# Performance work log

Hardware: AMD Instinct MI355X
Metric: run time of the kernel (lower is better)

## Reference

```python
import jax, jax.numpy as jnp
import numpy as np

D = 128  # chunk_embSize

def _mlp_one_layer(x, W, b):
    # MLP_one_layer in eval mode: dropout is identity -> tanh(x @ W^T + b)
    return jnp.tanh(x @ W.T + b)

def setup_inputs() -> dict:
    key = jax.random.key(0)
    ks = jax.random.split(key, 10)
    n_item, n_opi, n_user, L = 50000, 5000, 10000, 50
    s = 0.02  # initializer_range-style scale for linear weights
    return {
        "item_table": jax.random.normal(ks[0], (n_item, D), jnp.float32),
        "opin_table": jax.random.normal(ks[1], (n_opi, D), jnp.float32),
        "user_emb": jax.random.normal(ks[2], (n_user, D), jnp.float32),
        "attr_embedding": jax.random.normal(ks[3], (D,), jnp.float32),
        "Wq": jax.random.normal(ks[4], (D, D), jnp.float32) * s,
        "bq": jnp.zeros((D,), jnp.float32),
        "Wk": jax.random.normal(ks[5], (D, D), jnp.float32) * s,
        "bk": jnp.zeros((D,), jnp.float32),
        "Wv": jax.random.normal(ks[6], (D, D), jnp.float32) * s,
        "bv": jnp.zeros((D,), jnp.float32),
        "item_seqs": jax.random.randint(ks[7], (n_user, L), 0, n_item, jnp.int64),
        "opin_seqs": jax.random.randint(ks[8], (n_user, L), 0, n_opi, jnp.int64),
    }

def reference(item_table, opin_table, user_emb, attr_embedding,
              Wq, bq, Wk, bk, Wv, bv, item_seqs, opin_seqs):
    # FineRec UiMatrix.opin_update_ui (eval mode: all dropouts identity)
    item_emb = item_table[item_seqs]          # [U, L, D] gather
    opin_emb = opin_table[opin_seqs]          # [U, L, D] gather
    # k = k_layer(attr + item); v = v_layer(item + opin); q = q_layer(user)
    k_emb = _mlp_one_layer(attr_embedding[None, None, :] + item_emb, Wk, bk)
    v_emb = _mlp_one_layer(item_emb + opin_emb, Wv, bv)
    q_emb = _mlp_one_layer(user_emb, Wq, bq)  # [U, D]
    # unnormalized attention weights over the user's interaction sequence
    w_agg = jnp.einsum("ud,uld->ul", q_emb, k_emb)  # [U, L]
    mask = (item_seqs > 0).astype(w_agg.dtype)       # padding mask
    w_agg = w_agg * mask
    # weighted aggregation over sequence -> new user embedding
    user_embedding = jnp.einsum("ul,uld->ud", w_agg, v_emb)  # [U, D]
    return user_embedding
```

## Files before the change

kernel.cpp:

```cpp
#include <hip/hip_runtime.h>
#include <hip/hip_bf16.h>
#include <stdint.h>

typedef __attribute__((ext_vector_type(8))) short bf16x8;
typedef __attribute__((ext_vector_type(4))) float f32x4;

#define S_2LOG2E 2.8853900817779268f

#if __has_builtin(__builtin_amdgcn_exp2f)
#define EXP2F(x) __builtin_amdgcn_exp2f(x)
#else
#define EXP2F(x) __expf((x) * 0.6931471805599453f)
#endif
#if __has_builtin(__builtin_amdgcn_rcpf)
#define RCPF(x) __builtin_amdgcn_rcpf(x)
#else
#define RCPF(x) (1.0f / (x))
#endif

__device__ __forceinline__ float tanh_z(float z) {
    float e = EXP2F(z);
    float r = RCPF(e + 1.0f);
    return fmaf(-2.0f, r, 1.0f);
}
__device__ __forceinline__ float tanh_fast(float x) {
    float e = __expf(2.0f * x);
    return 1.0f - 2.0f / (e + 1.0f);
}

__device__ __forceinline__ bf16x8 pack2(float4 a, float4 b) {
    union { bf16x8 v; __hip_bfloat162 h[4]; } r;
    r.h[0] = __float22bfloat162_rn(make_float2(a.x, a.y));
    r.h[1] = __float22bfloat162_rn(make_float2(a.z, a.w));
    r.h[2] = __float22bfloat162_rn(make_float2(b.x, b.y));
    r.h[3] = __float22bfloat162_rn(make_float2(b.z, b.w));
    return r.v;
}
#define MFMA16(a, b, c) __builtin_amdgcn_mfma_f32_16x16x32_bf16((a), (b), (c), 0, 0, 0)

__global__ void finerec_prep(
    const float* __restrict__ user_emb, const float* __restrict__ attr,
    const float* __restrict__ Wq, const float* __restrict__ bq,
    const float* __restrict__ Wk, const float* __restrict__ bk,
    const float* __restrict__ Wv, const float* __restrict__ bv,
    const float* __restrict__ item_table, const float* __restrict__ opin_table,
    float* __restrict__ q_ws, float* __restrict__ bkz_ws, float* __restrict__ bvz_ws,
    short* __restrict__ wf_ws, short* __restrict__ itb, short* __restrict__ opb,
    float* __restrict__ out, int U, int n_item, int n_opi, int qb)
{
    const int bx = blockIdx.x, tid = threadIdx.x;
    if (bx >= qb + 49) {
        const int gid = (bx - qb - 49) * 256 + tid;
        const int stride = 224 * 256;
        const int tci = n_item * 16, tc = (n_item + n_opi) * 16;
        for (int c = gid; c < tc; c += stride) {
            if (c < tci) {
                const float* src = item_table + (size_t)c * 8;
                ((bf16x8*)itb)[c] = pack2(*(const float4*)src, *(const float4*)(src + 4));
            } else {
                const float* src = opin_table + (size_t)(c - tci) * 8;
                ((bf16x8*)opb)[c - tci] = pack2(*(const float4*)src, *(const float4*)(src + 4));
            }
        }
        return;
    }
    if (bx >= qb + 9) {
        const int gid = (bx - qb - 9) * 256 + tid;
        float4 z = {0.0f, 0.0f, 0.0f, 0.0f};
        for (int i = gid; i < U * 32; i += 40 * 256) ((float4*)out)[i] = z;
        return;
    }
    if (bx >= qb + 1) {
        const int bi = bx - qb - 1;
#pragma unroll
        for (int t = 0; t < 2; ++t) {
            const int g = bi * 512 + t * 256 + tid;
            const int mat = g >> 11, gg = g & 2047, r = gg >> 4, c = gg & 15;
            const float* src = (mat ? Wv : Wk) + r * 128 + c * 8;
            ((bf16x8*)wf_ws)[(mat << 11) + (r << 4) + (c ^ (r & 15))] =
                pack2(*(const float4*)src, *(const float4*)(src + 4));
        }
        return;
    }
    if (bx == qb) {
        if (tid < 128) {
            const float* wr = Wk + tid * 128;
            float s = bk[tid];
            for (int k = 0; k < 128; k += 4) {
                float4 w4 = *(const float4*)(wr + k);
                float4 a4 = *(const float4*)(attr + k);
                s += w4.x * a4.x + w4.y * a4.y + w4.z * a4.z + w4.w * a4.w;
            }
            bkz_ws[tid] = s * S_2LOG2E;
        } else if (tid < 256) {
            bvz_ws[tid - 128] = bv[tid - 128] * S_2LOG2E;
        }
        return;
    }
    const int wv = tid >> 6, lane = tid & 63;
    const int l15 = lane & 15, quad = lane >> 4;
    const int u0 = (bx * 4 + wv) * 16;
    int ur = u0 + l15; if (ur >= U) ur = U - 1;
    const float* up = user_emb + (size_t)ur * 128 + quad * 8;
    bf16x8 af[4];
#pragma unroll
    for (int ks = 0; ks < 4; ++ks)
        af[ks] = pack2(*(const float4*)(up + ks * 32), *(const float4*)(up + ks * 32 + 4));
#pragma unroll
    for (int nt = 0; nt < 8; ++nt) {
        const int n = nt * 16 + l15;
        const float* wp = Wq + n * 128 + quad * 8;
        f32x4 acc = {0, 0, 0, 0};
#pragma unroll
        for (int ks = 0; ks < 4; ++ks) {
            bf16x8 bf = pack2(*(const float4*)(wp + ks * 32), *(const float4*)(wp + ks * 32 + 4));
            acc = MFMA16(af[ks], bf, acc);
        }
        const float bqv = bq[n];
#pragma unroll
        for (int r = 0; r < 4; ++r) {
            int row = u0 + quad * 4 + r;
            if (row < U) q_ws[row * 128 + nt * 16 + l15] = tanh_fast(acc[r] + bqv);
        }
    }
}

template<int BF16>
__global__ __launch_bounds__(1024, 4) void finerec_main(
    const float* __restrict__ item_table, const float* __restrict__ opin_table,
    const int* __restrict__ item_seqs, const int* __restrict__ opin_seqs,
    const float* __restrict__ q_ws, const float* __restrict__ bkz_ws,
    const float* __restrict__ bvz_ws, const short* __restrict__ wf_ws,
    const short* __restrict__ itb, const short* __restrict__ opb,
    float* __restrict__ out, int U, int L)
{
    __shared__ __align__(16) short wlds[32768];
    __shared__ float q_lds[16 * 128];
    __shared__ float bkz_lds[128], bvz_lds[128];

    const int tid = threadIdx.x;
    const int wv = tid >> 6, lane = tid & 63, l15 = lane & 15, quad = lane >> 4;

    const bf16x8* wsrc = (const bf16x8*)wf_ws;
    bf16x8* wldsv = (bf16x8*)wlds;
#pragma unroll
    for (int i = 0; i < 4; ++i)
        wldsv[i * 1024 + tid] = wsrc[i * 1024 + tid];
    if (tid < 128)      bkz_lds[tid]       = bkz_ws[tid];
    else if (tid < 256) bvz_lds[tid - 128] = bvz_ws[tid - 128];
    __syncthreads();

    const int nwaves = gridDim.x * 16;
    const int njobs  = 4 * U;

#pragma unroll 1
    for (int job = blockIdx.x * 16 + wv; job < njobs; job += nwaves) {
        const int u  = job >> 2;
        const int rb = (job & 3) * 16;

        int vi = 0, vo = 0;
        if (lane < 16 && rb + lane < L) {
            vi = item_seqs[u * L + rb + lane];
            vo = opin_seqs[u * L + rb + lane];
        }
        const unsigned long long mb = __ballot(vi > 0);

        q_lds[wv * 128 + lane]      = q_ws[u * 128 + lane];
        q_lds[wv * 128 + 64 + lane] = q_ws[u * 128 + 64 + lane];

        const int idx = __shfl(vi, l15);
        bf16x8 ai[4];
        if (BF16) {
            const bf16x8* pb = (const bf16x8*)itb + (size_t)idx * 16 + quad;
#pragma unroll
            for (int ks = 0; ks < 4; ++ks) ai[ks] = pb[ks * 4];
        } else {
            const float* p = item_table + (size_t)idx * 128 + quad * 8;
#pragma unroll
            for (int ks = 0; ks < 4; ++ks)
                ai[ks] = pack2(*(const float4*)(p + ks * 32), *(const float4*)(p + ks * 32 + 4));
        }

        float w[4] = {0, 0, 0, 0};
#pragma unroll 1
        for (int nt = 0; nt < 8; ++nt) {
            const int n = nt * 16 + l15;
            f32x4 c = {0, 0, 0, 0};
#pragma unroll
            for (int ks = 0; ks < 4; ++ks)
                c = MFMA16(ai[ks], wldsv[(n << 4) + ((ks * 4 + quad) ^ (n & 15))], c);
            const float qv  = q_lds[wv * 128 + n];
            const float bkz = bkz_lds[n];
#pragma unroll
            for (int r = 0; r < 4; ++r)
                w[r] = fmaf(qv, tanh_z(fmaf(c[r], S_2LOG2E, bkz)), w[r]);
        }
#pragma unroll
        for (int r = 0; r < 4; ++r) {
            float t = w[r];
            t += __shfl_xor(t, 1); t += __shfl_xor(t, 2);
            t += __shfl_xor(t, 4); t += __shfl_xor(t, 8);
            w[r] = ((mb >> (quad * 4 + r)) & 1ull) ? t : 0.0f;
        }
        const int od = __shfl(vo, l15);
        bf16x8 ao[4];
        if (BF16) {
            const bf16x8* pb = (const bf16x8*)opb + (size_t)od * 16 + quad;
#pragma unroll
            for (int ks = 0; ks < 4; ++ks) ao[ks] = pb[ks * 4];
        } else {
            const float* p = opin_table + (size_t)od * 128 + quad * 8;
#pragma unroll
            for (int ks = 0; ks < 4; ++ks)
                ao[ks] = pack2(*(const float4*)(p + ks * 32), *(const float4*)(p + ks * 32 + 4));
        }
        float s0 = 0.0f, s1 = 0.0f;
#pragma unroll 1
        for (int nt = 0; nt < 8; ++nt) {
            const int n = nt * 16 + l15;
            f32x4 c = {0, 0, 0, 0};
#pragma unroll
            for (int ks = 0; ks < 4; ++ks) {
                bf16x8 wf = wldsv[2048 + (n << 4) + ((ks * 4 + quad) ^ (n & 15))];
                c = MFMA16(ai[ks], wf, c);
                c = MFMA16(ao[ks], wf, c);
            }
            const float bvz = bvz_lds[n];
            float acc = 0.0f;
#pragma unroll
            for (int r = 0; r < 4; ++r)
                acc = fmaf(w[r], tanh_z(fmaf(c[r], S_2LOG2E, bvz)), acc);
            acc += __shfl_xor(acc, 16);
            acc += __shfl_xor(acc, 32);
            const bool mine = (quad == (nt >> 1));
            s0 += (mine && !(nt & 1)) ? acc : 0.0f;
            s1 += (mine &&  (nt & 1)) ? acc : 0.0f;
        }
        atomicAdd(out + u * 128 + quad * 32 + l15, s0);
        atomicAdd(out + u * 128 + quad * 32 + 16 + l15, s1);
    }
}

extern "C" void kernel_launch(void* const* d_in, const int* in_sizes, int n_in,
                              void* d_out, int out_size, void* d_ws, size_t ws_size,
                              hipStream_t stream) {
    const float* item_table = (const float*)d_in[0];
    const float* opin_table = (const float*)d_in[1];
    const float* user_emb   = (const float*)d_in[2];
    const float* attr       = (const float*)d_in[3];
    const float* Wq = (const float*)d_in[4];
    const float* bq = (const float*)d_in[5];
    const float* Wk = (const float*)d_in[6];
    const float* bk = (const float*)d_in[7];
    const float* Wv = (const float*)d_in[8];
    const float* bv = (const float*)d_in[9];
    const int* item_seqs = (const int*)d_in[10];
    const int* opin_seqs = (const int*)d_in[11];
    float* out = (float*)d_out;

    const int U = in_sizes[2] / 128;
    const int L = in_sizes[10] / U;
    const int n_item = in_sizes[0] / 128;
    const int n_opi  = in_sizes[1] / 128;

    char* w = (char*)d_ws;
    float* q_ws   = (float*)w;               w += (size_t)U * 128 * 4;
    float* bkz_ws = (float*)w;               w += 512;
    float* bvz_ws = (float*)w;               w += 512;
    short* wf_ws  = (short*)w;               w += 4096 * 16;
    short* itb    = (short*)w;               w += (size_t)n_item * 128 * 2;
    short* opb    = (short*)w;               w += (size_t)n_opi * 128 * 2;
    const size_t need = (size_t)(w - (char*)d_ws);
    const int use_bf16 = (ws_size >= need) ? 1 : 0;

    const int qb = (U + 63) / 64;
    const int prep_grid = qb + 49 + (use_bf16 ? 224 : 0);
    finerec_prep<<<prep_grid, 256, 0, stream>>>(
        user_emb, attr, Wq, bq, Wk, bk, Wv, bv, item_table, opin_table,
        q_ws, bkz_ws, bvz_ws, wf_ws, itb, opb, out, U, n_item, n_opi, qb);

    if (use_bf16)
        finerec_main<1><<<512, 1024, 0, stream>>>(
            item_table, opin_table, item_seqs, opin_seqs,
            q_ws, bkz_ws, bvz_ws, wf_ws, itb, opb, out, U, L);
    else
        finerec_main<0><<<512, 1024, 0, stream>>>(
            item_table, opin_table, item_seqs, opin_seqs,
            q_ws, bkz_ws, bvz_ws, wf_ws, itb, opb, out, U, L);
}
```

Baseline: 186.9 us.

## Pack sequence rows densely across users, fold scaling into weights and bias init

Jobs now cover 16 consecutive flattened (user, position) rows instead of 16-row blocks per user. With L=50 the old scheme padded to 64 rows, so about 22% of the MFMA/tanh work was wasted. A job that straddles two users takes a split path that selects q per row and issues separate atomics for each user. The 2*log2(e) scale is folded into the bf16 weights and the bias is preloaded as the MFMA accumulator, dropping per-element FMAs. The q staging through LDS is removed, the cast grid is sized to the table, and L=50 gets a compile-time specialization.

New measurement: 179.1 us, median of 2. 4.2% less time.

```diff
diff --git a/kernel.cpp b/kernel.cpp
--- a/kernel.cpp
+++ b/kernel.cpp
@@ -35,6 +35,10 @@
     r.h[2] = __float22bfloat162_rn(make_float2(b.x, b.y));
     r.h[3] = __float22bfloat162_rn(make_float2(b.z, b.w));
     return r.v;
+}
+__device__ __forceinline__ float4 scl4(float4 a) {
+    a.x *= S_2LOG2E; a.y *= S_2LOG2E; a.z *= S_2LOG2E; a.w *= S_2LOG2E;
+    return a;
 }
 #define MFMA16(a, b, c) __builtin_amdgcn_mfma_f32_16x16x32_bf16((a), (b), (c), 0, 0, 0)
 
@@ -50,8 +54,9 @@
 {
     const int bx = blockIdx.x, tid = threadIdx.x;
     if (bx >= qb + 49) {
+        const int castb = gridDim.x - qb - 49;
         const int gid = (bx - qb - 49) * 256 + tid;
-        const int stride = 224 * 256;
+        const int stride = castb * 256;
         const int tci = n_item * 16, tc = (n_item + n_opi) * 16;
         for (int c = gid; c < tc; c += stride) {
             if (c < tci) {
@@ -78,7 +83,7 @@
             const int mat = g >> 11, gg = g & 2047, r = gg >> 4, c = gg & 15;
             const float* src = (mat ? Wv : Wk) + r * 128 + c * 8;
             ((bf16x8*)wf_ws)[(mat << 11) + (r << 4) + (c ^ (r & 15))] =
-                pack2(*(const float4*)src, *(const float4*)(src + 4));
+                pack2(scl4(*(const float4*)src), scl4(*(const float4*)(src + 4)));
         }
         return;
     }
@@ -125,19 +130,19 @@
     }
 }
 
-template<int BF16>
+template<int BF16, int LC>
 __global__ __launch_bounds__(1024, 4) void finerec_main(
     const float* __restrict__ item_table, const float* __restrict__ opin_table,
     const int* __restrict__ item_seqs, const int* __restrict__ opin_seqs,
     const float* __restrict__ q_ws, const float* __restrict__ bkz_ws,
     const float* __restrict__ bvz_ws, const short* __restrict__ wf_ws,
     const short* __restrict__ itb, const short* __restrict__ opb,
-    float* __restrict__ out, int U, int L)
+    float* __restrict__ out, int U, int Lrt)
 {
     __shared__ __align__(16) short wlds[32768];
-    __shared__ float q_lds[16 * 128];
     __shared__ float bkz_lds[128], bvz_lds[128];
 
+    const int L = LC ? LC : Lrt;
     const int tid = threadIdx.x;
     const int wv = tid >> 6, lane = tid & 63, l15 = lane & 15, quad = lane >> 4;
 
@@ -150,23 +155,23 @@
     else if (tid < 256) bvz_lds[tid - 128] = bvz_ws[tid - 128];
     __syncthreads();
 
+    const int UL = U * L;
+    const int njobs = (UL + 15) >> 4;
     const int nwaves = gridDim.x * 16;
-    const int njobs  = 4 * U;
 
 #pragma unroll 1
     for (int job = blockIdx.x * 16 + wv; job < njobs; job += nwaves) {
-        const int u  = job >> 2;
-        const int rb = (job & 3) * 16;
+        const int g0 = job << 4;
+        const int uA = g0 / L;
+        const int bb = L - (g0 - uA * L);
+        const bool split = (bb < 16) && (uA + 1 < U);
 
         int vi = 0, vo = 0;
-        if (lane < 16 && rb + lane < L) {
-            vi = item_seqs[u * L + rb + lane];
-            vo = opin_seqs[u * L + rb + lane];
+        if (lane < 16 && g0 + lane < UL) {
+            vi = item_seqs[g0 + lane];
+            vo = opin_seqs[g0 + lane];
         }
         const unsigned long long mb = __ballot(vi > 0);
-
-        q_lds[wv * 128 + lane]      = q_ws[u * 128 + lane];
-        q_lds[wv * 128 + 64 + lane] = q_ws[u * 128 + 64 + lane];
 
         const int idx = __shfl(vi, l15);
         bf16x8 ai[4];
@@ -181,19 +186,41 @@
                 ai[ks] = pack2(*(const float4*)(p + ks * 32), *(const float4*)(p + ks * 32 + 4));
         }
 
+        const float* qpA = q_ws + (size_t)uA * 128;
         float w[4] = {0, 0, 0, 0};
-#pragma unroll 1
-        for (int nt = 0; nt < 8; ++nt) {
-            const int n = nt * 16 + l15;
-            f32x4 c = {0, 0, 0, 0};
-#pragma unroll
-            for (int ks = 0; ks < 4; ++ks)
-                c = MFMA16(ai[ks], wldsv[(n << 4) + ((ks * 4 + quad) ^ (n & 15))], c);
-            const float qv  = q_lds[wv * 128 + n];
-            const float bkz = bkz_lds[n];
-#pragma unroll
-            for (int r = 0; r < 4; ++r)
-                w[r] = fmaf(qv, tanh_z(fmaf(c[r], S_2LOG2E, bkz)), w[r]);
+
+        if (!split) {
+#pragma unroll 1
+            for (int nt = 0; nt < 8; ++nt) {
+                const int n = nt * 16 + l15;
+                const float qa = qpA[n];
+                const float bz = bkz_lds[n];
+                f32x4 c = {bz, bz, bz, bz};
+#pragma unroll
+                for (int ks = 0; ks < 4; ++ks)
+                    c = MFMA16(ai[ks], wldsv[(n << 4) + ((ks * 4 + quad) ^ l15)], c);
+#pragma unroll
+                for (int r = 0; r < 4; ++r)
+                    w[r] = fmaf(qa, tanh_z(c[r]), w[r]);
+            }
+        } else {
+            const float* qpB = qpA + 128;
+#pragma unroll 1
+            for (int nt = 0; nt < 8; ++nt) {
+                const int n = nt * 16 + l15;
+                const float qa = qpA[n];
+                const float qb2 = qpB[n];
+                const float bz = bkz_lds[n];
+                f32x4 c = {bz, bz, bz, bz};
+#pragma unroll
+                for (int ks = 0; ks < 4; ++ks)
+                    c = MFMA16(ai[ks], wldsv[(n << 4) + ((ks * 4 + quad) ^ l15)], c);
+#pragma unroll
+                for (int r = 0; r < 4; ++r) {
+                    const float qv = (quad * 4 + r < bb) ? qa : qb2;
+                    w[r] = fmaf(qv, tanh_z(c[r]), w[r]);
+                }
+            }
         }
 #pragma unroll
         for (int r = 0; r < 4; ++r) {
@@ -214,30 +241,67 @@
             for (int ks = 0; ks < 4; ++ks)
                 ao[ks] = pack2(*(const float4*)(p + ks * 32), *(const float4*)(p + ks * 32 + 4));
         }
-        float s0 = 0.0f, s1 = 0.0f;
-#pragma unroll 1
-        for (int nt = 0; nt < 8; ++nt) {
-            const int n = nt * 16 + l15;
-            f32x4 c = {0, 0, 0, 0};
-#pragma unroll
-            for (int ks = 0; ks < 4; ++ks) {
-                bf16x8 wf = wldsv[2048 + (n << 4) + ((ks * 4 + quad) ^ (n & 15))];
-                c = MFMA16(ai[ks], wf, c);
-                c = MFMA16(ao[ks], wf, c);
-            }
-            const float bvz = bvz_lds[n];
-            float acc = 0.0f;
-#pragma unroll
-            for (int r = 0; r < 4; ++r)
-                acc = fmaf(w[r], tanh_z(fmaf(c[r], S_2LOG2E, bvz)), acc);
-            acc += __shfl_xor(acc, 16);
-            acc += __shfl_xor(acc, 32);
-            const bool mine = (quad == (nt >> 1));
-            s0 += (mine && !(nt & 1)) ? acc : 0.0f;
-            s1 += (mine &&  (nt & 1)) ? acc : 0.0f;
-        }
-        atomicAdd(out + u * 128 + quad * 32 + l15, s0);
-        atomicAdd(out + u * 128 + quad * 32 + 16 + l15, s1);
+        float* op = out + (size_t)uA * 128 + quad * 32 + l15;
+        if (!split) {
+            float s0 = 0.0f, s1 = 0.0f;
+#pragma unroll 1
+            for (int nt = 0; nt < 8; ++nt) {
+                const int n = nt * 16 + l15;
+                const float bz = bvz_lds[n];
+                f32x4 c = {bz, bz, bz, bz};
+#pragma unroll
+                for (int ks = 0; ks < 4; ++ks) {
+                    const bf16x8 wf = wldsv[2048 + (n << 4) + ((ks * 4 + quad) ^ l15)];
+                    c = MFMA16(ai[ks], wf, c);
+                    c = MFMA16(ao[ks], wf, c);
+                }
+                float acc = 0.0f;
+#pragma unroll
+                for (int r = 0; r < 4; ++r)
+                    acc = fmaf(w[r], tanh_z(c[r]), acc);
+                acc += __shfl_xor(acc, 16);
+                acc += __shfl_xor(acc, 32);
+                const bool mine = (quad == (nt >> 1));
+                s0 += (mine && !(nt & 1)) ? acc : 0.0f;
+                s1 += (mine &&  (nt & 1)) ? acc : 0.0f;
+            }
+            atomicAdd(op, s0);
+            atomicAdd(op + 16, s1);
+        } else {
+            float sA0 = 0.0f, sA1 = 0.0f, sB0 = 0.0f, sB1 = 0.0f;
+#pragma unroll 1
+            for (int nt = 0; nt < 8; ++nt) {
+                const int n = nt * 16 + l15;
+                const float bz = bvz_lds[n];
+                f32x4 c = {bz, bz, bz, bz};
+#pragma unroll
+                for (int ks = 0; ks < 4; ++ks) {
+                    const bf16x8 wf = wldsv[2048 + (n << 4) + ((ks * 4 + quad) ^ l15)];
+                    c = MFMA16(ai[ks], wf, c);
+                    c = MFMA16(ao[ks], wf, c);
+                }
+                float accT = 0.0f, accA = 0.0f;
+#pragma unroll
+                for (int r = 0; r < 4; ++r) {
+                    const float t = w[r] * tanh_z(c[r]);
+                    accT += t;
+                    accA += (quad * 4 + r < bb) ? t : 0.0f;
+                }
+                accT += __shfl_xor(accT, 16); accT += __shfl_xor(accT, 32);
+                accA += __shfl_xor(accA, 16); accA += __shfl_xor(accA, 32);
+                const float accB = accT - accA;
+                const bool mine = (quad == (nt >> 1));
+                const bool lo = !(nt & 1);
+                sA0 += (mine && lo)  ? accA : 0.0f;
+                sA1 += (mine && !lo) ? accA : 0.0f;
+                sB0 += (mine && lo)  ? accB : 0.0f;
+                sB1 += (mine && !lo) ? accB : 0.0f;
+            }
+            atomicAdd(op, sA0);
+            atomicAdd(op + 16, sA1);
+            atomicAdd(op + 128, sB0);
+            atomicAdd(op + 144, sB1);
+        }
     }
 }
 
@@ -274,17 +338,29 @@
     const int use_bf16 = (ws_size >= need) ? 1 : 0;
 
     const int qb = (U + 63) / 64;
-    const int prep_grid = qb + 49 + (use_bf16 ? 224 : 0);
+    const int castb = use_bf16 ? (((n_item + n_opi) * 16 + 255) / 256) : 0;
+    const int prep_grid = qb + 49 + castb;
     finerec_prep<<<prep_grid, 256, 0, stream>>>(
         user_emb, attr, Wq, bq, Wk, bk, Wv, bv, item_table, opin_table,
         q_ws, bkz_ws, bvz_ws, wf_ws, itb, opb, out, U, n_item, n_opi, qb);
 
-    if (use_bf16)
-        finerec_main<1><<<512, 1024, 0, stream>>>(
-            item_table, opin_table, item_seqs, opin_seqs,
-            q_ws, bkz_ws, bvz_ws, wf_ws, itb, opb, out, U, L);
-    else
-        finerec_main<0><<<512, 1024, 0, stream>>>(
-            item_table, opin_table, item_seqs, opin_seqs,
-            q_ws, bkz_ws, bvz_ws, wf_ws, itb, opb, out, U, L);
-}
+    if (use_bf16) {
+        if (L == 50)
+            finerec_main<1, 50><<<512, 1024, 0, stream>>>(
+                item_table, opin_table, item_seqs, opin_seqs,
+                q_ws, bkz_ws, bvz_ws, wf_ws, itb, opb, out, U, L);
+        else
+            finerec_main<1, 0><<<512, 1024, 0, stream>>>(
+                item_table, opin_table, item_seqs, opin_seqs,
+                q_ws, bkz_ws, bvz_ws, wf_ws, itb, opb, out, U, L);
+    } else {
+        if (L == 50)
+            finerec_main<0, 50><<<512, 1024, 0, stream>>>(
+                item_table, opin_table, item_seqs, opin_seqs,
+                q_ws, bkz_ws, bvz_ws, wf_ws, itb, opb, out, U, L);
+        else
+            finerec_main<0, 0><<<512, 1024, 0, stream>>>(
+                item_table, opin_table, item_seqs, opin_seqs,
+                q_ws, bkz_ws, bvz_ws, wf_ws, itb, opb, out, U, L);
+    }
+}
```
